# Kernel tuning notes

Measured on AMD Instinct MI355X. Metric: run time of the kernel, lower is better.

## Reference

```python
import jax, jax.numpy as jnp
import numpy as np
jax.config.update("jax_enable_x64", True)

B, T, EPROJS, ODIM, U = 16, 1600, 512, 2048, 200
RISK_FACTOR = 0.1
NEG = float('-inf')


def _safe_lse0(x):
    # logsumexp over axis 0, safe for all -inf columns (no NaN in fwd or bwd)
    m = jnp.max(x, axis=0)
    ms = jnp.where(jnp.isinf(m), 0.0, m)
    s = jnp.sum(jnp.exp(x - ms), axis=0)
    out = ms + jnp.log(jnp.where(s == 0, 1.0, s))
    return jnp.where(s == 0, NEG, out)


def _log_sub_exp(a, b):
    # faithful port of log_substraction_exp: log(exp(a) - exp(b))
    mask1 = (~jnp.isinf(a)) & (~jnp.isinf(b))
    a_ = jnp.where(mask1, a, -1.0)
    b_ = jnp.where(mask1, b, -2.0)
    tmp = b_ + jnp.log(jnp.exp(a_ - b_) - 1.0)
    a_ = jnp.where(jnp.isinf(tmp), -2000.0, a_)
    b_ = jnp.where(jnp.isinf(tmp), -2001.0, b_)
    ans1 = b_ + jnp.log(jnp.exp(a_ - b_) - 1.0)
    ans = jnp.where(mask1, ans1, NEG)
    ans = jnp.where((~jnp.isinf(a)) & jnp.isinf(b), a, ans)
    return ans


def _ctc_bayes_loss(hs_pad, W, bvec, hlens, ys_pad):
    Bn, Tn, _ = hs_pad.shape
    Un = ys_pad.shape[1]
    S = 2 * Un + 1  # extended CTC state count (blank-interleaved)
    logits = hs_pad @ W.T + bvec
    logprob = jax.nn.log_softmax(logits, axis=-1).astype(jnp.float64)  # [B,T,V]
    ysc = jnp.where(ys_pad < 0, 0, ys_pad)
    olens = jnp.sum(ys_pad >= 0, axis=1)
    lp_blank = logprob[:, :, 0]                                        # [B,T]
    lp_label = jnp.take_along_axis(logprob, ysc[:, None, :], axis=2)   # [B,T,U]
    # emission log-probs on extended states: even=blank, odd=label u=(s-1)//2
    pair = jnp.stack([jnp.broadcast_to(lp_blank[:, :, None], (Bn, Tn, Un)), lp_label], axis=-1).reshape(Bn, Tn, 2 * Un)
    em = jnp.concatenate([pair, lp_blank[:, :, None]], axis=-1)        # [B,T,S]
    # skip transition (s-2 -> s) allowed into odd s with differing neighbor label
    allow_odd = jnp.concatenate([jnp.zeros((Bn, 1), bool), ysc[:, 1:] != ysc[:, :-1]], axis=1)
    allow = jnp.concatenate([jnp.stack([jnp.zeros((Bn, Un), bool), allow_odd], -1).reshape(Bn, 2 * Un), jnp.zeros((Bn, 1), bool)], axis=1)
    allow_fwd = jnp.concatenate([allow[:, 2:], jnp.zeros((Bn, 2), bool)], axis=1)
    em_t = jnp.transpose(em, (1, 0, 2))                                # [T,B,S]
    ninf2 = jnp.full((Bn, S), NEG, jnp.float64)
    alpha0 = ninf2.at[:, 0].set(em_t[0, :, 0]).at[:, 1].set(em_t[0, :, 1])

    def alpha_step(carry, e):
        s1 = jnp.concatenate([jnp.full((Bn, 1), NEG, jnp.float64), carry[:, :-1]], 1)
        s2 = jnp.concatenate([jnp.full((Bn, 2), NEG, jnp.float64), carry[:, :-2]], 1)
        s2 = jnp.where(allow, s2, NEG)
        new = e + _safe_lse0(jnp.stack([carry, s1, s2], 0))
        return new, new

    _, alpha_rest = jax.lax.scan(alpha_step, alpha0, em_t[1:])
    alpha_all = jnp.concatenate([alpha0[None], alpha_rest], 0)         # [T,B,S]

    sidx = jnp.arange(S)[None, :]
    fin = jnp.where((sidx == 2 * olens[:, None]) | (sidx == 2 * olens[:, None] - 1), 0.0, NEG)
    em_nxt = jnp.concatenate([em_t[1:], em_t[-1:]], 0)                 # em_nxt[t] = em_t[t+1]
    ts = jnp.arange(Tn - 1, -1, -1)

    def beta_step(carry, x):
        t, e_next = x
        g = e_next + carry
        g1 = jnp.concatenate([g[:, 1:], jnp.full((Bn, 1), NEG, jnp.float64)], 1)
        g2 = jnp.concatenate([g[:, 2:], jnp.full((Bn, 2), NEG, jnp.float64)], 1)
        g2 = jnp.where(allow_fwd, g2, NEG)
        new = _safe_lse0(jnp.stack([g, g1, g2], 0))
        new = jnp.where((t == hlens - 1)[:, None], fin, new)
        return new, new

    _, beta_rev = jax.lax.scan(beta_step, ninf2, (ts, em_nxt[::-1]))
    beta_all = beta_rev[::-1]                                          # [T,B,S]

    alpha_u = jnp.transpose(alpha_all, (1, 2, 0))[:, 1::2, :]          # [B,U,T]
    beta_u = jnp.transpose(beta_all, (1, 2, 0))[:, 1::2, :]
    valid = (jnp.arange(Un)[None, :, None] < olens[:, None, None]) & (jnp.arange(Tn)[None, None, :] < hlens[:, None, None])
    alpha_u = jnp.where(valid, alpha_u, NEG)
    beta_u = jnp.where(valid, beta_u, NEG)
    p = jnp.where(valid, jnp.transpose(lp_label, (0, 2, 1)), NEG)      # [B,U,T]
    beta_prime = jnp.concatenate([_log_sub_exp(beta_u[:, :, :-1], beta_u[:, :, 1:] + p[:, :, 1:]), beta_u[:, :, -1:]], axis=-1)
    risk = jnp.arange(1, Tn + 1, dtype=jnp.float64)[None, None, :] / hlens[:, None, None].astype(jnp.float64) * RISK_FACTOR
    loss_state = alpha_u + beta_prime + risk
    loss_state = jnp.where(jnp.isnan(loss_state), NEG, loss_state)
    # aggregate == 'time': logsumexp over t, pick last valid label position
    m = jnp.max(loss_state, axis=2)
    ms = jnp.where(jnp.isinf(m), 0.0, m)
    ssum = jnp.sum(jnp.exp(loss_state - ms[:, :, None]), axis=2)
    loss_u = jnp.where(ssum == 0, NEG, ms + jnp.log(jnp.where(ssum == 0, 1.0, ssum)))
    mask = jnp.isinf(loss_u)
    last = jnp.sum(~mask, axis=1) - 1
    loss_fsas = loss_u[jnp.arange(Bn), last]
    loss_fsas = jnp.where(hlens < olens, 0.0, loss_fsas)
    return jnp.mean(-loss_fsas)


def setup_inputs() -> dict:
    key = jax.random.key(0)
    k1, k2, k3, k4, k5, k6 = jax.random.split(key, 6)
    hs_pad = jax.random.normal(k1, (B, T, EPROJS), jnp.float32)
    W = jax.random.normal(k2, (ODIM, EPROJS), jnp.float32) * 0.05
    b = jnp.zeros((ODIM,), jnp.float32)
    hlens = (T - jax.random.randint(k3, (B,), 0, 200)).astype(jnp.int64)
    ys = jax.random.randint(k4, (B, U), 1, ODIM)
    olens = U - jax.random.randint(k5, (B,), 0, 20)
    ys_pad = jnp.where(jnp.arange(U)[None, :] < olens[:, None], ys, -1).astype(jnp.int64)
    ali = jax.random.randint(k6, (B, U), 0, T).astype(jnp.int64)
    return {"hs_pad": hs_pad, "W": W, "b": b, "hlens": hlens, "ys_pad": ys_pad, "ali": ali}


def reference(hs_pad, W, b, hlens, ys_pad, ali):
    # ali is unused for risk_strategy='time' (matches the torch module)
    return _ctc_bayes_loss(hs_pad, W, b, hlens, ys_pad)
```

## Files before the change

kernel.cpp:

```cpp
#include <hip/hip_runtime.h>
#include <math.h>


#define Bn    16
#define Tn    1600
#define NE    512
#define OD    2048
#define Un    200
#define Sn    401
#define NLAB  201
#define NGC   256
#define LPS   256

#define NEGINF (-INFINITY)
#define LSE_SUB_CONST_F (-2000.4586715f)

typedef short bf8_t  __attribute__((ext_vector_type(8)));
typedef float f32x4  __attribute__((ext_vector_type(4)));

__device__ __forceinline__ unsigned short f2bf(float x) {
    unsigned int u = __float_as_uint(x);
    unsigned int r = (u + 0x7FFFu + ((u >> 16) & 1u)) >> 16;
    return (unsigned short)r;
}
__device__ __forceinline__ void lse_merge_v(float& M, float& S, float v) {
    if (v > M) { S = S * __expf(M - v) + 1.f; M = v; }
    else       { S += __expf(v - M); }
}
__device__ __forceinline__ void lse_merge_ms(float& M, float& S, float m2, float s2) {
    if (s2 > 0.f) {
        if (m2 > M) { S = S * __expf(M - m2) + s2; M = m2; }
        else        { S += s2 * __expf(m2 - M); }
    }
}

__global__ __launch_bounds__(256)
void cast_hs_kernel(const float* __restrict__ src, unsigned short* __restrict__ dst, int n8) {
    int i = blockIdx.x * 256 + threadIdx.x;
    if (i >= n8) return;
    const float4* s4 = (const float4*)(src + (size_t)i * 8);
    float4 a = s4[0], b = s4[1];
    uint4 o;
    o.x = f2bf(a.x) | ((unsigned)f2bf(a.y) << 16);
    o.y = f2bf(a.z) | ((unsigned)f2bf(a.w) << 16);
    o.z = f2bf(b.x) | ((unsigned)f2bf(b.y) << 16);
    o.w = f2bf(b.z) | ((unsigned)f2bf(b.w) << 16);
    *(uint4*)(dst + (size_t)i * 8) = o;
}

__global__ __launch_bounds__(64)
void gather_kernel(const float* __restrict__ W, const float* __restrict__ bias,
                   const int* __restrict__ ys, unsigned short* __restrict__ Wgb,
                   float* __restrict__ biasg)
{
    const int b = blockIdx.x, j = blockIdx.y, tid = threadIdx.x;
    int col = -1;
    if (j == 0) col = 0;
    else if (j <= Un) { int y = ys[b * Un + j - 1]; col = (y < 0) ? 0 : y; }
    unsigned short* dst = Wgb + ((size_t)b * NGC + j) * NE;
    if (col >= 0) {
        const float* srcc = W + (size_t)col * NE;
        #pragma unroll
        for (int it = 0; it < 8; ++it) dst[tid + it * 64] = f2bf(srcc[tid + it * 64]);
    } else {
        #pragma unroll
        for (int it = 0; it < 8; ++it) dst[tid + it * 64] = 0;
    }
    if (tid == 0) biasg[b * NGC + j] = (col >= 0) ? bias[col] : 0.f;
}

#define KCH  64
#define ASTR 72

__global__ __launch_bounds__(256, 2)
void gemm_main_kernel(const unsigned short* __restrict__ hsb,
                      const unsigned short* __restrict__ Wb,
                      const float* __restrict__ bias,
                      float* __restrict__ Pm, float* __restrict__ Ps)
{
    __shared__ union {
        struct { unsigned short A[128 * ASTR]; unsigned short B[128 * ASTR]; } t;
        struct { float m[128 * 33]; float s[128 * 33]; } r;
    } sh;
    const int tid  = threadIdx.x;
    const int lane = tid & 63, w = tid >> 6;
    const int mw = w & 1, nw = w >> 1;
    const int quad = lane >> 4, lc = lane & 15;
    const int row0 = blockIdx.x * 128;
    const int c0   = blockIdx.y * 128;

    f32x4 acc[4][4];
    #pragma unroll
    for (int mi = 0; mi < 4; ++mi)
        #pragma unroll
        for (int ni = 0; ni < 4; ++ni) acc[mi][ni] = (f32x4)0.f;

    for (int kc = 0; kc < NE / KCH; ++kc) {
        __syncthreads();
        #pragma unroll
        for (int i = 0; i < 4; ++i) {
            int idx = tid + i * 256;
            int r = idx >> 3, c8 = idx & 7;
            *(uint4*)&sh.t.A[r * ASTR + c8 * 8] =
                *(const uint4*)&hsb[(size_t)(row0 + r) * NE + kc * KCH + c8 * 8];
            *(uint4*)&sh.t.B[r * ASTR + c8 * 8] =
                *(const uint4*)&Wb[(size_t)(c0 + r) * NE + kc * KCH + c8 * 8];
        }
        __syncthreads();
        #pragma unroll
        for (int ks = 0; ks < 2; ++ks) {
            bf8_t af[4], bg[4];
            #pragma unroll
            for (int mi = 0; mi < 4; ++mi)
                af[mi] = *(const bf8_t*)&sh.t.A[(mw * 64 + mi * 16 + lc) * ASTR + ks * 32 + quad * 8];
            #pragma unroll
            for (int ni = 0; ni < 4; ++ni)
                bg[ni] = *(const bf8_t*)&sh.t.B[(nw * 64 + ni * 16 + lc) * ASTR + ks * 32 + quad * 8];
            #pragma unroll
            for (int mi = 0; mi < 4; ++mi)
                #pragma unroll
                for (int ni = 0; ni < 4; ++ni)
                    acc[mi][ni] = __builtin_amdgcn_mfma_f32_16x16x32_bf16(af[mi], bg[ni], acc[mi][ni], 0, 0, 0);
        }
    }
    __syncthreads();
    float bcol[4];
    #pragma unroll
    for (int ni = 0; ni < 4; ++ni) bcol[ni] = bias[c0 + nw * 64 + ni * 16 + lc];
    #pragma unroll
    for (int mi = 0; mi < 4; ++mi)
        #pragma unroll
        for (int r = 0; r < 4; ++r) {
            float M = NEGINF, S = 0.f;
            #pragma unroll
            for (int ni = 0; ni < 4; ++ni) lse_merge_v(M, S, acc[mi][ni][r] + bcol[ni]);
            int rl = mw * 64 + mi * 16 + quad * 4 + r;
            sh.r.m[rl * 33 + nw * 16 + lc] = M;
            sh.r.s[rl * 33 + nw * 16 + lc] = S;
        }
    __syncthreads();
    if (tid < 128) {
        float M = NEGINF, S = 0.f;
        #pragma unroll 4
        for (int j = 0; j < 32; ++j) lse_merge_ms(M, S, sh.r.m[tid * 33 + j], sh.r.s[tid * 33 + j]);
        Pm[(size_t)blockIdx.y * 25600 + row0 + tid] = M;
        Ps[(size_t)blockIdx.y * 25600 + row0 + tid] = S;
    }
}

__global__ __launch_bounds__(256)
void lse_reduce_kernel(const float* __restrict__ Pm, const float* __restrict__ Ps,
                       float* __restrict__ lse)
{
    int row = blockIdx.x * 256 + threadIdx.x;
    float M = NEGINF, S = 0.f;
    #pragma unroll 4
    for (int nt = 0; nt < 16; ++nt)
        lse_merge_ms(M, S, Pm[(size_t)nt * 25600 + row], Ps[(size_t)nt * 25600 + row]);
    lse[row] = M + logf(S);
}

__global__ __launch_bounds__(256, 2)
void gemm_label_kernel(const unsigned short* __restrict__ hsb,
                       const unsigned short* __restrict__ Wgb,
                       const float* __restrict__ biasg, const float* __restrict__ lse,
                       float* __restrict__ lpl, float* __restrict__ lpbk)
{
    __shared__ unsigned short shA[64 * ASTR];
    __shared__ unsigned short shB[128 * ASTR];
    const int tid  = threadIdx.x;
    const int lane = tid & 63, w = tid >> 6;
    const int mw = w & 1, nw = w >> 1;
    const int quad = lane >> 4, lc = lane & 15;
    const int b  = blockIdx.x / 25, mt = blockIdx.x % 25;
    const int r0 = b * Tn + mt * 64;
    const int c0 = blockIdx.y * 128;

    f32x4 acc[2][4];
    #pragma unroll
    for (int mi = 0; mi < 2; ++mi)
        #pragma unroll
        for (int ni = 0; ni < 4; ++ni) acc[mi][ni] = (f32x4)0.f;

    const unsigned short* Wgbb = Wgb + (size_t)b * NGC * NE;
    for (int kc = 0; kc < NE / KCH; ++kc) {
        __syncthreads();
        #pragma unroll
        for (int i = 0; i < 2; ++i) {
            int idx = tid + i * 256;
            int r = idx >> 3, c8 = idx & 7;
            *(uint4*)&shA[r * ASTR + c8 * 8] =
                *(const uint4*)&hsb[(size_t)(r0 + r) * NE + kc * KCH + c8 * 8];
        }
        #pragma unroll
        for (int i = 0; i < 4; ++i) {
            int idx = tid + i * 256;
            int r = idx >> 3, c8 = idx & 7;
            *(uint4*)&shB[r * ASTR + c8 * 8] =
                *(const uint4*)&Wgbb[(size_t)(c0 + r) * NE + kc * KCH + c8 * 8];
        }
        __syncthreads();
        #pragma unroll
        for (int ks = 0; ks < 2; ++ks) {
            bf8_t af[2], bg[4];
            #pragma unroll
            for (int mi = 0; mi < 2; ++mi)
                af[mi] = *(const bf8_t*)&shA[(mw * 32 + mi * 16 + lc) * ASTR + ks * 32 + quad * 8];
            #pragma unroll
            for (int ni = 0; ni < 4; ++ni)
                bg[ni] = *(const bf8_t*)&shB[(nw * 64 + ni * 16 + lc) * ASTR + ks * 32 + quad * 8];
            #pragma unroll
            for (int mi = 0; mi < 2; ++mi)
                #pragma unroll
                for (int ni = 0; ni < 4; ++ni)
                    acc[mi][ni] = __builtin_amdgcn_mfma_f32_16x16x32_bf16(af[mi], bg[ni], acc[mi][ni], 0, 0, 0);
        }
    }
    #pragma unroll
    for (int mi = 0; mi < 2; ++mi)
        #pragma unroll
        for (int r = 0; r < 4; ++r) {
            int row = r0 + mw * 32 + mi * 16 + quad * 4 + r;
            float lsv = lse[row];
            #pragma unroll
            for (int ni = 0; ni < 4; ++ni) {
                int col = c0 + nw * 64 + ni * 16 + lc;
                float v = acc[mi][ni][r] + biasg[b * NGC + col] - lsv;
                if (col == 0)          lpbk[row] = v;
                else if (col < NLAB)   lpl[(size_t)row * LPS + (col - 1)] = v;
                else                   lpl[(size_t)row * LPS + (col - 1)] = 0.f;
            }
        }
}

#define IDX(s) ((s) + 2)

__device__ __forceinline__ float lse2f(float a, float b) {
    float mx = fmaxf(a, b);
    if (isinf(mx)) return NEGINF;
    return mx + __logf(__expf(a - mx) + __expf(b - mx));
}
__device__ __forceinline__ float lse3f(float v0, float v1, float v2) {
    float mx = fmaxf(v0, fmaxf(v1, v2));
    if (isinf(mx)) return NEGINF;
    return mx + __logf(__expf(v0 - mx) + __expf(v1 - mx) + __expf(v2 - mx));
}

#define STEP_BAR() do { \
    asm volatile("s_waitcnt lgkmcnt(0)" ::: "memory"); \
    __builtin_amdgcn_s_barrier(); \
    __builtin_amdgcn_sched_barrier(0); \
} while (0)

__global__ __launch_bounds__(256)
void scan_kernel(const float* __restrict__ lpl, const float* __restrict__ lpbk,
                 const int* __restrict__ hlens, const int* __restrict__ ys,
                 float* __restrict__ ast, float* __restrict__ bst)
{
    __shared__ float buf[2][408];
    __shared__ float ebs[Tn];
    __shared__ int   sh_olen, sh_hlen;

    const int b    = blockIdx.x & (Bn - 1);
    const int role = blockIdx.x >> 4;
    const int tid  = threadIdx.x;

    if (tid == 0) {
        int o = 0;
        for (int u = 0; u < Un; u++) if (ys[b * Un + u] >= 0) o++;
        sh_olen = o;
        sh_hlen = hlens[b];
    }
    for (int idx = tid; idx < 408; idx += 256) {
        buf[0][idx] = NEGINF;
        buf[1][idx] = NEGINF;
    }
    const float* lpbb = lpbk + (size_t)b * Tn;
    for (int i = tid; i < Tn; i += 256) ebs[i] = lpbb[i];

    bool a1allow = false;
    if (tid >= 1 && tid < Un) {
        int y0 = ys[b * Un + tid - 1]; if (y0 < 0) y0 = 0;
        int y1 = ys[b * Un + tid];     if (y1 < 0) y1 = 0;
        a1allow = (y0 != y1);
    }
    bool a2allow = false;
    if (tid + 1 >= 1 && tid + 1 < Un) {
        int y0 = ys[b * Un + tid];     if (y0 < 0) y0 = 0;
        int y1 = ys[b * Un + tid + 1]; if (y1 < 0) y1 = 0;
        a2allow = (y0 != y1);
    }
    __syncthreads();

    const float* lplb = lpl + (size_t)b * Tn * LPS;
    const int s0 = 2 * tid, s1 = 2 * tid + 1;
    const bool v0ok = (s0 < Sn);
    const bool v1ok = (s1 < Sn);
    const int  olen = sh_olen, hlen = sh_hlen;
    const int  ustar = olen - 1;

    if (role == 0) {
        float* as = ast + (size_t)b * Tn;
        if (tid == 0) { buf[0][IDX(0)] = ebs[0]; buf[0][IDX(1)] = lplb[0]; }
        if (tid == ustar) as[0] = (tid == 0) ? lplb[0] : NEGINF;
        __syncthreads();

        #define ASTEP(T, EO) do { \
            const float* cur = buf[((T) - 1) & 1]; \
            float* nxt = buf[(T) & 1]; \
            if (v0ok) { \
                float c1 = cur[IDX(s0) - 1]; \
                float c2 = cur[IDX(s0)], c3 = cur[IDX(s1)]; \
                float nv0 = lse2f(c2, c1) + ebs[T]; \
                nxt[IDX(s0)] = nv0; \
                if (v1ok) { \
                    float a1v2 = a1allow ? c1 : NEGINF; \
                    float nv1 = lse3f(c3, c2, a1v2) + (EO); \
                    nxt[IDX(s1)] = nv1; \
                    if (tid == ustar) as[T] = nv1; \
                } \
            } \
            STEP_BAR(); \
        } while (0)

        float eoA = lplb[(size_t)1 * LPS + tid];
        float eoB = lplb[(size_t)2 * LPS + tid];
        for (int t = 1; t < Tn; t += 2) {
            int rA = t + 2; if (rA > Tn - 1) rA = Tn - 1;
            float nA = lplb[(size_t)rA * LPS + tid];
            ASTEP(t, eoA); eoA = nA;
            if (t + 1 < Tn) {
                int rB = t + 3; if (rB > Tn - 1) rB = Tn - 1;
                float nB = lplb[(size_t)rB * LPS + tid];
                ASTEP(t + 1, eoB); eoB = nB;
            }
        }
        #undef ASTEP
    } else {
        float* bs = bst + (size_t)b * Tn;

        #define BSTEP(T, E0, E1) do { \
            const int it = (Tn - 1 - (T)) & 1; \
            const float* cur = buf[it]; \
            float* nxt = buf[it ^ 1]; \
            float eb = ebs[((T) + 1 > Tn - 1) ? (Tn - 1) : ((T) + 1)]; \
            if (v0ok) { \
                float c0 = cur[IDX(s0)],     c1 = cur[IDX(s0) + 1]; \
                float c2 = cur[IDX(s0) + 2], c3 = cur[IDX(s0) + 3]; \
                float g0e = eb + c0; \
                float g1e = (E0) + c1; \
                float nv0 = lse2f(g0e, g1e); \
                float g0o = (E0) + c1; \
                float g1o = eb + c2; \
                float g2o = a2allow ? ((E1) + c3) : NEGINF; \
                float mh = fmaxf(g1o, g2o); \
                float h = NEGINF; \
                if (!isinf(mh)) \
                    h = mh + __logf(__expf(g1o - mh) + __expf(g2o - mh)); \
                float nv1 = v1ok ? lse3f(g0o, g1o, g2o) : NEGINF; \
                if ((T) == hlen - 1) { \
                    nv0 = (s0 == 2 * olen || s0 == 2 * olen - 1) ? 0.f : NEGINF; \
                    nv1 = (s1 == 2 * olen || s1 == 2 * olen - 1) ? 0.f : NEGINF; \
                } \
                nxt[IDX(s0)] = nv0; \
                if (v1ok) { \
                    nxt[IDX(s1)] = nv1; \
                    if (tid == ustar) { \
                        float bp; \
                        if ((T) >= hlen)          bp = NEGINF; \
                        else if ((T) == hlen - 1) bp = 0.f;  \
                        else if (isinf(g0o))      bp = h; \
                        else if (isinf(h))        bp = LSE_SUB_CONST_F; \
                        else { \
                            float sumlog = h - g0o; \
                            int k = (int)((__float_as_uint(fabsf(g0o)) >> 23) & 0xFF) - 127 - 53; \
                            if (k < -53) k = -53; \
                            bp = (sumlog > 709.7827f || sumlog < 0.69314718f * (float)k) \
                                 ? LSE_SUB_CONST_F : h; \
                        } \
                        bs[T] = bp; \
                    } \
                } \
            } \
            STEP_BAR(); \
        } while (0)

        float e0A = lplb[(size_t)(Tn - 1) * LPS + tid];
        float e1A = lplb[(size_t)(Tn - 1) * LPS + tid + 1];
        float e0B = e0A, e1B = e1A;
        for (int t = Tn - 1; t > 0; t -= 2) {
            int rA = t - 1;
            float n0A = lplb[(size_t)rA * LPS + tid];
            float n1A = lplb[(size_t)rA * LPS + tid + 1];
            BSTEP(t, e0A, e1A);
            e0A = n0A; e1A = n1A;

            int rB = t - 2; if (rB < 0) rB = 0;
            float n0B = lplb[(size_t)rB * LPS + tid];
            float n1B = lplb[(size_t)rB * LPS + tid + 1];
            BSTEP(t - 1, e0B, e1B);
            e0B = n0B; e1B = n1B;
        }
        #undef BSTEP
    }
}

#define TCH 8
#define TPC (Tn / TCH)

__global__ __launch_bounds__(64)
void loss_kernel(const int* __restrict__ hlens, const int* __restrict__ ys,
                 const float* __restrict__ ast, const float* __restrict__ bst,
                 float* __restrict__ lossb)
{
    const int b = blockIdx.x, tid = threadIdx.x;
    __shared__ float sm[TCH], ss[TCH];
    __shared__ int sh_olen;
    if (tid == 0) {
        int o = 0;
        for (int u = 0; u < Un; u++) if (ys[b * Un + u] >= 0) o++;
        sh_olen = o;
    }
    __syncthreads();
    const int hlen = hlens[b];
    const float risk_c = 0.1f / (float)hlen;
    if (tid < TCH) {
        float m = NEGINF, s = 0.f;
        const float* as = ast + (size_t)b * Tn;
        const float* bs = bst + (size_t)b * Tn;
        const int t0 = tid * TPC, t1 = t0 + TPC;
        for (int t = t0; t < t1; ++t) {
            float v = as[t] + bs[t] + (float)(t + 1) * risk_c;
            if (!isinf(v)) lse_merge_v(m, s, v);
        }
        sm[tid] = m; ss[tid] = s;
    }
    __syncthreads();
    if (tid == 0) {
        float M = NEGINF, S = 0.f;
        #pragma unroll
        for (int c = 0; c < TCH; ++c) lse_merge_ms(M, S, sm[c], ss[c]);
        float lf = (S == 0.f) ? NEGINF : M + __logf(S);
        if (hlen < sh_olen) lf = 0.f;
        lossb[b] = lf;
    }
}

__global__ void finalize_kernel(const float* __restrict__ lossb, float* __restrict__ out) {
    if (threadIdx.x == 0 && blockIdx.x == 0) {
        float ssum = 0.f;
        for (int i = 0; i < Bn; i++) ssum += lossb[i];
        out[0] = -ssum / (float)Bn;
    }
}

extern "C" void kernel_launch(void* const* d_in, const int* in_sizes, int n_in,
                              void* d_out, int out_size, void* d_ws, size_t ws_size,
                              hipStream_t stream) {
    const float* hs    = (const float*)d_in[0];
    const float* W     = (const float*)d_in[1];
    const float* bias  = (const float*)d_in[2];
    const int*   hlens = (const int*)d_in[3];
    const int*   ys    = (const int*)d_in[4];
    float* out = (float*)d_out;

    char* p = (char*)d_ws;
    float* lpl    = (float*)p;  p += (size_t)25601 * LPS * 4;
    float* lpbk   = (float*)p;  p += (size_t)25600 * 4;
    unsigned short* hsb = (unsigned short*)p; p += (size_t)25600 * NE * 2;
    unsigned short* Wb  = (unsigned short*)p; p += (size_t)OD * NE * 2;
    unsigned short* Wgb = (unsigned short*)p; p += (size_t)Bn * NGC * NE * 2;
    float* Pm    = (float*)p;   p += (size_t)16 * 25600 * 4;
    float* Ps    = (float*)p;   p += (size_t)16 * 25600 * 4;
    float* lse   = (float*)p;   p += (size_t)25600 * 4;
    float* biasg = (float*)p;   p += (size_t)Bn * NGC * 4;
    float* ast   = (float*)p;   p += (size_t)Bn * Tn * 4;
    float* bst   = (float*)p;   p += (size_t)Bn * Tn * 4;
    float* lossb = (float*)p;   p += 256;

    hipLaunchKernelGGL(cast_hs_kernel, dim3(6400), dim3(256), 0, stream,
                       hs, hsb, 25600 * NE / 8);
    hipLaunchKernelGGL(cast_hs_kernel, dim3(512), dim3(256), 0, stream,
                       W, Wb, OD * NE / 8);
    hipLaunchKernelGGL(gather_kernel, dim3(Bn, NGC), dim3(64), 0, stream,
                       W, bias, ys, Wgb, biasg);
    hipLaunchKernelGGL(gemm_main_kernel, dim3(200, 16), dim3(256), 0, stream,
                       hsb, Wb, bias, Pm, Ps);
    hipLaunchKernelGGL(lse_reduce_kernel, dim3(100), dim3(256), 0, stream,
                       Pm, Ps, lse);
    hipLaunchKernelGGL(gemm_label_kernel, dim3(400, 2), dim3(256), 0, stream,
                       hsb, Wgb, biasg, lse, lpl, lpbk);
    hipLaunchKernelGGL(scan_kernel, dim3(2 * Bn), dim3(256), 0, stream,
                       lpl, lpbk, hlens, ys, ast, bst);
    hipLaunchKernelGGL(loss_kernel, dim3(Bn), dim3(64), 0, stream,
                       hlens, ys, ast, bst, lossb);
    hipLaunchKernelGGL(finalize_kernel, dim3(1), dim3(64), 0, stream, lossb, out);
}
```

Measured before the change: 1.202 ms.

## Stage per-step emission rows into LDS via double-buffered async global_load_lds windows

Replaces the per-step register prefetch of emission log-probs in the alpha/beta scan kernel with double-buffered 16-timestep windows. Each window is copied into shared memory with global_load_lds DMA, and the next window is fetched while the current one is consumed. The aim is to take global-memory latency off the serial, barrier-bound recurrence. In exchange it adds about 32KB of LDS per block and a full vmcnt wait plus barrier at each window boundary.

```diff
diff --git a/kernel.cpp b/kernel.cpp
--- a/kernel.cpp
+++ b/kernel.cpp
@@ -11,6 +11,8 @@
 #define NLAB  201
 #define NGC   256
 #define LPS   256
+#define WS    16
+#define NW    100
 
 #define NEGINF (-INFINITY)
 #define LSE_SUB_CONST_F (-2000.4586715f)
@@ -251,6 +253,11 @@
     __builtin_amdgcn_s_barrier(); \
     __builtin_amdgcn_sched_barrier(0); \
 } while (0)
+#define WIN_BAR() do { \
+    asm volatile("s_waitcnt vmcnt(0) lgkmcnt(0)" ::: "memory"); \
+    __builtin_amdgcn_s_barrier(); \
+    __builtin_amdgcn_sched_barrier(0); \
+} while (0)
 
 __global__ __launch_bounds__(256)
 void scan_kernel(const float* __restrict__ lpl, const float* __restrict__ lpbk,
@@ -259,11 +266,13 @@
 {
     __shared__ float buf[2][408];
     __shared__ float ebs[Tn];
+    __shared__ float em[2][WS][LPS];
     __shared__ int   sh_olen, sh_hlen;
 
     const int b    = blockIdx.x & (Bn - 1);
     const int role = blockIdx.x >> 4;
     const int tid  = threadIdx.x;
+    const int wid  = tid >> 6, lane = tid & 63;
 
     if (tid == 0) {
         int o = 0;
@@ -290,12 +299,31 @@
         int y1 = ys[b * Un + tid + 1]; if (y1 < 0) y1 = 0;
         a2allow = (y0 != y1);
     }
-    __syncthreads();
 
     const float* lplb = lpl + (size_t)b * Tn * LPS;
     const int s0 = 2 * tid, s1 = 2 * tid + 1;
     const bool v0ok = (s0 < Sn);
     const bool v1ok = (s1 < Sn);
+
+    auto dma_window = [&](int k, int bufi) {
+        #pragma unroll
+        for (int m = 0; m < 4; ++m) {
+            int i = 4 * wid + m;
+            int j = WS * k + i;
+            int r = role ? (1600 - j) : (j + 1);
+            if (r > Tn - 1) r = Tn - 1;
+            __builtin_amdgcn_global_load_lds(
+                (const __attribute__((address_space(1))) unsigned int*)
+                    &lplb[(size_t)r * LPS + 4 * lane],
+                (__attribute__((address_space(3))) unsigned int*)
+                    &em[bufi][i][0],
+                16, 0, 0);
+        }
+    };
+
+    dma_window(0, 0);
+    __syncthreads();
+
     const int  olen = sh_olen, hlen = sh_hlen;
     const int  ustar = olen - 1;
 
@@ -303,105 +331,92 @@
         float* as = ast + (size_t)b * Tn;
         if (tid == 0) { buf[0][IDX(0)] = ebs[0]; buf[0][IDX(1)] = lplb[0]; }
         if (tid == ustar) as[0] = (tid == 0) ? lplb[0] : NEGINF;
-        __syncthreads();
-
-        #define ASTEP(T, EO) do { \
-            const float* cur = buf[((T) - 1) & 1]; \
-            float* nxt = buf[(T) & 1]; \
-            if (v0ok) { \
-                float c1 = cur[IDX(s0) - 1]; \
-                float c2 = cur[IDX(s0)], c3 = cur[IDX(s1)]; \
-                float nv0 = lse2f(c2, c1) + ebs[T]; \
-                nxt[IDX(s0)] = nv0; \
-                if (v1ok) { \
-                    float a1v2 = a1allow ? c1 : NEGINF; \
-                    float nv1 = lse3f(c3, c2, a1v2) + (EO); \
-                    nxt[IDX(s1)] = nv1; \
-                    if (tid == ustar) as[T] = nv1; \
-                } \
-            } \
-            STEP_BAR(); \
-        } while (0)
-
-        float eoA = lplb[(size_t)1 * LPS + tid];
-        float eoB = lplb[(size_t)2 * LPS + tid];
-        for (int t = 1; t < Tn; t += 2) {
-            int rA = t + 2; if (rA > Tn - 1) rA = Tn - 1;
-            float nA = lplb[(size_t)rA * LPS + tid];
-            ASTEP(t, eoA); eoA = nA;
-            if (t + 1 < Tn) {
-                int rB = t + 3; if (rB > Tn - 1) rB = Tn - 1;
-                float nB = lplb[(size_t)rB * LPS + tid];
-                ASTEP(t + 1, eoB); eoB = nB;
+        WIN_BAR();
+
+        for (int k = 0; k < NW; ++k) {
+            const int cb = k & 1;
+            if (k + 1 < NW) dma_window(k + 1, cb ^ 1);
+            for (int i = 0; i < WS; ++i) {
+                const int t = WS * k + i + 1;
+                if (t < Tn) {
+                    const float* cur = buf[(t - 1) & 1];
+                    float* nxt = buf[t & 1];
+                    if (v0ok) {
+                        float eo = em[cb][i][tid];
+                        float c1 = cur[IDX(s0) - 1];
+                        float c2 = cur[IDX(s0)], c3 = cur[IDX(s1)];
+                        float nv0 = lse2f(c2, c1) + ebs[t];
+                        nxt[IDX(s0)] = nv0;
+                        if (v1ok) {
+                            float a1v2 = a1allow ? c1 : NEGINF;
+                            float nv1 = lse3f(c3, c2, a1v2) + eo;
+                            nxt[IDX(s1)] = nv1;
+                            if (tid == ustar) as[t] = nv1;
+                        }
+                    }
+                    STEP_BAR();
+                }
             }
-        }
-        #undef ASTEP
+            WIN_BAR();
+        }
     } else {
         float* bs = bst + (size_t)b * Tn;
-
-        #define BSTEP(T, E0, E1) do { \
-            const int it = (Tn - 1 - (T)) & 1; \
-            const float* cur = buf[it]; \
-            float* nxt = buf[it ^ 1]; \
-            float eb = ebs[((T) + 1 > Tn - 1) ? (Tn - 1) : ((T) + 1)]; \
-            if (v0ok) { \
-                float c0 = cur[IDX(s0)],     c1 = cur[IDX(s0) + 1]; \
-                float c2 = cur[IDX(s0) + 2], c3 = cur[IDX(s0) + 3]; \
-                float g0e = eb + c0; \
-                float g1e = (E0) + c1; \
-                float nv0 = lse2f(g0e, g1e); \
-                float g0o = (E0) + c1; \
-                float g1o = eb + c2; \
-                float g2o = a2allow ? ((E1) + c3) : NEGINF; \
-                float mh = fmaxf(g1o, g2o); \
-                float h = NEGINF; \
-                if (!isinf(mh)) \
-                    h = mh + __logf(__expf(g1o - mh) + __expf(g2o - mh)); \
-                float nv1 = v1ok ? lse3f(g0o, g1o, g2o) : NEGINF; \
-                if ((T) == hlen - 1) { \
-                    nv0 = (s0 == 2 * olen || s0 == 2 * olen - 1) ? 0.f : NEGINF; \
-                    nv1 = (s1 == 2 * olen || s1 == 2 * olen - 1) ? 0.f : NEGINF; \
-                } \
-                nxt[IDX(s0)] = nv0; \
-                if (v1ok) { \
-                    nxt[IDX(s1)] = nv1; \
-                    if (tid == ustar) { \
-                        float bp; \
-                        if ((T) >= hlen)          bp = NEGINF; \
-                        else if ((T) == hlen - 1) bp = 0.f;  \
-                        else if (isinf(g0o))      bp = h; \
-                        else if (isinf(h))        bp = LSE_SUB_CONST_F; \
-                        else { \
-                            float sumlog = h - g0o; \
-                            int k = (int)((__float_as_uint(fabsf(g0o)) >> 23) & 0xFF) - 127 - 53; \
-                            if (k < -53) k = -53; \
-                            bp = (sumlog > 709.7827f || sumlog < 0.69314718f * (float)k) \
-                                 ? LSE_SUB_CONST_F : h; \
-                        } \
-                        bs[T] = bp; \
-                    } \
-                } \
-            } \
-            STEP_BAR(); \
-        } while (0)
-
-        float e0A = lplb[(size_t)(Tn - 1) * LPS + tid];
-        float e1A = lplb[(size_t)(Tn - 1) * LPS + tid + 1];
-        float e0B = e0A, e1B = e1A;
-        for (int t = Tn - 1; t > 0; t -= 2) {
-            int rA = t - 1;
-            float n0A = lplb[(size_t)rA * LPS + tid];
-            float n1A = lplb[(size_t)rA * LPS + tid + 1];
-            BSTEP(t, e0A, e1A);
-            e0A = n0A; e1A = n1A;
-
-            int rB = t - 2; if (rB < 0) rB = 0;
-            float n0B = lplb[(size_t)rB * LPS + tid];
-            float n1B = lplb[(size_t)rB * LPS + tid + 1];
-            BSTEP(t - 1, e0B, e1B);
-            e0B = n0B; e1B = n1B;
-        }
-        #undef BSTEP
+        WIN_BAR();
+
+        for (int k = 0; k < NW; ++k) {
+            const int cb = k & 1;
+            if (k + 1 < NW) dma_window(k + 1, cb ^ 1);
+            for (int i = 0; i < WS; ++i) {
+                const int j = WS * k + i;
+                const int T = Tn - 1 - j;
+                const int it = j & 1;
+                const float* cur = buf[it];
+                float* nxt = buf[it ^ 1];
+                float eb = ebs[(T + 1 > Tn - 1) ? (Tn - 1) : (T + 1)];
+                if (v0ok) {
+                    float e0 = em[cb][i][tid];
+                    float e1 = em[cb][i][tid + 1];
+                    float c0 = cur[IDX(s0)],     c1 = cur[IDX(s0) + 1];
+                    float c2 = cur[IDX(s0) + 2], c3 = cur[IDX(s0) + 3];
+                    float g0e = eb + c0;
+                    float g1e = e0 + c1;
+                    float nv0 = lse2f(g0e, g1e);
+                    float g0o = e0 + c1;
+                    float g1o = eb + c2;
+                    float g2o = a2allow ? (e1 + c3) : NEGINF;
+                    float mh = fmaxf(g1o, g2o);
+                    float h = NEGINF;
+                    if (!isinf(mh))
+                        h = mh + __logf(__expf(g1o - mh) + __expf(g2o - mh));
+                    float nv1 = v1ok ? lse3f(g0o, g1o, g2o) : NEGINF;
+                    if (T == hlen - 1) {
+                        nv0 = (s0 == 2 * olen || s0 == 2 * olen - 1) ? 0.f : NEGINF;
+                        nv1 = (s1 == 2 * olen || s1 == 2 * olen - 1) ? 0.f : NEGINF;
+                    }
+                    nxt[IDX(s0)] = nv0;
+                    if (v1ok) {
+                        nxt[IDX(s1)] = nv1;
+                        if (tid == ustar) {
+                            float bp;
+                            if (T >= hlen)          bp = NEGINF;
+                            else if (T == hlen - 1) bp = 0.f;
+                            else if (isinf(g0o))    bp = h;
+                            else if (isinf(h))      bp = LSE_SUB_CONST_F;
+                            else {
+                                float sumlog = h - g0o;
+                                int kk = (int)((__float_as_uint(fabsf(g0o)) >> 23) & 0xFF) - 127 - 53;
+                                if (kk < -53) kk = -53;
+                                bp = (sumlog > 709.7827f || sumlog < 0.69314718f * (float)kk)
+                                     ? LSE_SUB_CONST_F : h;
+                            }
+                            bs[T] = bp;
+                        }
+                    }
+                }
+                STEP_BAR();
+            }
+            WIN_BAR();
+        }
     }
 }
 
```

Result: no change. 1.208 ms (+0.5%).
